# Optimization experiments

Measured on AMD Instinct MI355X. Metric: run time of the kernel, lower is better.

## Reference

```python
import jax, jax.numpy as jnp
import numpy as np

HEADS = 2

def gat_layer(x, edge_index, W, att, bias):
    # x: [N, Fin], W: [H*C, Fin], att: [1, H, 2C], bias: [C]
    N = x.shape[0]
    C = bias.shape[0]
    # add self loops (source_to_target: x_j from row 0, aggregate onto row 1)
    loop = jnp.arange(N, dtype=edge_index.dtype)
    src = jnp.concatenate([edge_index[0], loop])
    dst = jnp.concatenate([edge_index[1], loop])
    h = (x @ W.T).reshape(N, HEADS, C)          # [N, H, C]
    x_j = h[src]                                 # [E, H, C]
    x_i = h[dst]                                 # [E, H, C]
    x_cat = jnp.concatenate([x_i, x_j], axis=-1) # [E, H, 2C]
    alpha = (x_cat * att).sum(-1)                # [E, H]
    alpha = jnp.where(alpha >= 0, alpha, 0.2 * alpha)  # leaky_relu(0.2)
    # NOTE: module uses a global (not per-destination) normalization
    alpha = jnp.exp(alpha - alpha.max())
    alpha = alpha / (alpha.sum(axis=0, keepdims=True) + 1e-10)
    msg = x_j * alpha[..., None]                 # [E, H, C]
    aggr = jax.ops.segment_sum(msg, dst, num_segments=N)  # [N, H, C]
    return aggr.mean(axis=1) + bias              # [N, C]

def setup_inputs() -> dict:
    key = jax.random.key(0)
    ks = jax.random.split(key, 7)
    N, Fin, C = 50000, 128, 64
    E = 800000
    x = jax.random.normal(ks[0], (N, Fin), dtype=jnp.float32)
    edge_index = jax.random.randint(ks[1], (2, E), 0, N, dtype=jnp.int64)
    W1 = jax.random.normal(ks[2], (HEADS * C, Fin), dtype=jnp.float32) * 0.05
    att1 = jax.random.normal(ks[3], (1, HEADS, 2 * C), dtype=jnp.float32) * 0.05
    b1 = jnp.zeros((C,), dtype=jnp.float32)
    W2 = jax.random.normal(ks[4], (HEADS * C, C), dtype=jnp.float32) * 0.05
    att2 = jax.random.normal(ks[5], (1, HEADS, 2 * C), dtype=jnp.float32) * 0.05
    b2 = jnp.zeros((C,), dtype=jnp.float32)
    return {"x": x, "edge_index": edge_index, "W1": W1, "att1": att1,
            "b1": b1, "W2": W2, "att2": att2, "b2": b2}

def reference(x, edge_index, W1, att1, b1, W2, att2, b2):
    h = gat_layer(x, edge_index, W1, att1, b1)
    h = jax.nn.relu(h)
    # F.dropout with training flag: treated as eval (identity) for determinism
    out = gat_layer(h, edge_index, W2, att2, b2)
    return out
```

## Files before the change

kernel.cpp:

```cpp
#include <hip/hip_runtime.h>
#include <hip/hip_bf16.h>
#include <math.h>


#define HP 8
#define HG 64
#define NHISTB (HP * HG)
#define HRANGE_MAX 6272
#define NSELF 16
#define NWGT  256

using short8 = __attribute__((ext_vector_type(8))) short;
using f32x4  = __attribute__((ext_vector_type(4))) float;

__device__ __forceinline__ unsigned f2bf(float x) {
  unsigned u = __float_as_uint(x);
  return (u + 0x7fffu + ((u >> 16) & 1u)) >> 16;
}
__device__ __forceinline__ float bflo(unsigned p) { return __uint_as_float(p << 16); }
__device__ __forceinline__ float bfhi(unsigned p) { return __uint_as_float(p & 0xffff0000u); }
__device__ __forceinline__ float lrexp(float a) {
  a = a >= 0.f ? a : 0.2f * a;
  return __expf(a);
}

__device__ __forceinline__ void block_zadd(float z0, float z1,
                                           float* __restrict__ Zp) {
  __shared__ float r0[16], r1[16];
  int lane = threadIdx.x & 63, w = threadIdx.x >> 6;
  int nw = blockDim.x >> 6;
#pragma unroll
  for (int off = 32; off; off >>= 1) {
    z0 += __shfl_down(z0, off, 64);
    z1 += __shfl_down(z1, off, 64);
  }
  if (lane == 0) { r0[w] = z0; r1[w] = z1; }
  __syncthreads();
  if (threadIdx.x == 0) {
    float s0 = 0.f, s1 = 0.f;
    for (int i = 0; i < nw; ++i) { s0 += r0[i]; s1 += r1[i]; }
    atomicAdd(&Zp[0], s0);
    atomicAdd(&Zp[1], s1);
  }
}

__global__ __launch_bounds__(256) void init_ws(
    const float* __restrict__ W1, const float* __restrict__ W2,
    unsigned short* __restrict__ wbf1, unsigned short* __restrict__ wbf2,
    float* __restrict__ Z, int* __restrict__ flags) {
  int tid = blockIdx.x * 256 + threadIdx.x;
  int stride = gridDim.x * 256;
  for (int i = tid; i < 128 * 128; i += stride)
    wbf1[i] = (unsigned short)f2bf(W1[i]);
  for (int i = tid; i < 128 * 64; i += stride)
    wbf2[i] = (unsigned short)f2bf(W2[i]);
  if (tid < 4) Z[tid] = 0.f;
  if (tid < 64) flags[tid] = -1;
}

template <int FIN, bool AB16>
__global__ __launch_bounds__(256) void gemm_mfma(
    const void* __restrict__ xin, const unsigned short* __restrict__ Wb,
    const float* __restrict__ att, unsigned* __restrict__ hq,
    float* __restrict__ si, float* __restrict__ sj,
    int N,
    const int* __restrict__ dstE, unsigned short* __restrict__ partial,
    int E, int nhistb, int hstep, int eper) {
  const int tid = threadIdx.x;

  constexpr int WB = 128 * FIN * 2;
  constexpr int SMEM = (WB > HRANGE_MAX * 4) ? WB : HRANGE_MAX * 4;
  __shared__ __align__(16) unsigned char smem[SMEM];

  if ((int)blockIdx.x < nhistb) {
    int* lhist = (int*)smem;
    const int p = blockIdx.x & (HP - 1);
    const int g = blockIdx.x >> 3;
    const int lo = p * hstep;
    for (int i = tid; i < hstep; i += 256) lhist[i] = 0;
    __syncthreads();
    const int eb = g * eper;
    const int ee = min(E, eb + eper);
    int e = eb + tid;
    for (; e + 3 * 256 < ee; e += 4 * 256) {
      int d0 = dstE[e] - lo;
      int d1 = dstE[e + 256] - lo;
      int d2 = dstE[e + 2 * 256] - lo;
      int d3 = dstE[e + 3 * 256] - lo;
      if ((unsigned)d0 < (unsigned)hstep) atomicAdd(&lhist[d0], 1);
      if ((unsigned)d1 < (unsigned)hstep) atomicAdd(&lhist[d1], 1);
      if ((unsigned)d2 < (unsigned)hstep) atomicAdd(&lhist[d2], 1);
      if ((unsigned)d3 < (unsigned)hstep) atomicAdd(&lhist[d3], 1);
    }
    for (; e < ee; e += 256) {
      int d = dstE[e] - lo;
      if ((unsigned)d < (unsigned)hstep) atomicAdd(&lhist[d], 1);
    }
    __syncthreads();
    for (int i = tid; i < hstep; i += 256) {
      int node = lo + i;
      if (node < N) partial[(size_t)g * N + node] = (unsigned short)lhist[i];
    }
    return;
  }

  constexpr int KS = FIN / 32;
  constexpr int CPR = FIN / 8;
  constexpr int NCHUNK = 128 * CPR;

  unsigned short* wlds = (unsigned short*)smem;

  const int w    = tid >> 6;
  const int lane = tid & 63;
  const int cl   = lane & 15;
  const int grp  = lane >> 4;
  const int n0   = (blockIdx.x - nhistb) * 64;

  const int arow = n0 + w * 16 + cl;
  const bool avalid = arow < N;

  short8 afrag[KS];
#pragma unroll
  for (int ks = 0; ks < KS; ++ks) {
    if constexpr (AB16) {
      short8 z = {0, 0, 0, 0, 0, 0, 0, 0};
      afrag[ks] = z;
      if (avalid) {
        const unsigned short* xb = (const unsigned short*)xin;
        afrag[ks] =
            *(const short8*)(xb + (size_t)arow * FIN + ks * 32 + grp * 8);
      }
    } else {
      float4 v0 = make_float4(0.f, 0.f, 0.f, 0.f), v1 = v0;
      if (avalid) {
        const float* xf = (const float*)xin;
        const float4* xp =
            (const float4*)(xf + (size_t)arow * FIN + ks * 32 + grp * 8);
        v0 = xp[0];
        v1 = xp[1];
      }
      union { short8 s8; unsigned u[4]; } af;
      af.u[0] = f2bf(v0.x) | (f2bf(v0.y) << 16);
      af.u[1] = f2bf(v0.z) | (f2bf(v0.w) << 16);
      af.u[2] = f2bf(v1.x) | (f2bf(v1.y) << 16);
      af.u[3] = f2bf(v1.z) | (f2bf(v1.w) << 16);
      afrag[ks] = af.s8;
    }
  }

  const uint4* Wb4 = (const uint4*)Wb;
  for (int c = tid; c < NCHUNK; c += 256) {
    int row = c / CPR;
    int cc  = c & (CPR - 1);
    *(uint4*)&wlds[row * FIN + ((cc ^ (row & (CPR - 1))) * 8)] = Wb4[c];
  }
  __syncthreads();

  f32x4 acc[8];
#pragma unroll
  for (int ct = 0; ct < 8; ++ct) acc[ct] = (f32x4){0.f, 0.f, 0.f, 0.f};

  const int swz = cl & (CPR - 1);
#pragma unroll
  for (int ks = 0; ks < KS; ++ks) {
#pragma unroll
    for (int ct = 0; ct < 8; ++ct) {
      const unsigned short* bp =
          &wlds[(ct * 16 + cl) * FIN + (((ks * 4 + grp) ^ swz) * 8)];
      short8 bfrag = *(const short8*)bp;
      acc[ct] = __builtin_amdgcn_mfma_f32_16x16x32_bf16(afrag[ks], bfrag,
                                                        acc[ct], 0, 0, 0);
    }
  }

  float ai[8], aj[8];
#pragma unroll
  for (int ct = 0; ct < 8; ++ct) {
    int hd = ct >> 2;
    int cw = (ct & 3) * 16 + cl;
    ai[ct] = att[hd * 128 + cw];
    aj[ct] = att[hd * 128 + 64 + cw];
  }

#pragma unroll
  for (int r = 0; r < 4; ++r) {
    int node = n0 + w * 16 + grp * 4 + r;
    float s0i = 0.f, s0j = 0.f, s1i = 0.f, s1j = 0.f;
    unsigned wpk[4];
#pragma unroll
    for (int ct = 0; ct < 4; ++ct) {
      float v0 = acc[ct][r];
      float v1 = acc[ct + 4][r];
      s0i += v0 * ai[ct];
      s0j += v0 * aj[ct];
      s1i += v1 * ai[ct + 4];
      s1j += v1 * aj[ct + 4];
      wpk[ct] = f2bf(v0) | (f2bf(v1) << 16);
    }
#pragma unroll
    for (int off = 8; off; off >>= 1) {
      s0i += __shfl_xor(s0i, off, 64);
      s0j += __shfl_xor(s0j, off, 64);
      s1i += __shfl_xor(s1i, off, 64);
      s1j += __shfl_xor(s1j, off, 64);
    }
    if (node < N) {
#pragma unroll
      for (int ct = 0; ct < 4; ++ct)
        hq[(size_t)node * 64 + ct * 16 + cl] = wpk[ct];
      if (cl == 0) {
        si[node * 2 + 0] = s0i;
        si[node * 2 + 1] = s1i;
        sj[node * 2 + 0] = s0j;
        sj[node * 2 + 1] = s1j;
      }
    }
  }
}

__global__ __launch_bounds__(256) void scan_full(
    unsigned short* __restrict__ partial, int* __restrict__ rowptr,
    int* __restrict__ flags, int N, int Eall, int nb) {
  __shared__ int ts[256];
  __shared__ int pre_s;
  const int b = blockIdx.x, t = threadIdx.x;
  const int base = b * 1024 + t * 4;
  int r0 = 0, r1 = 0, r2 = 0, r3 = 0;
  if (base < N) {
#pragma unroll 8
    for (int g = 0; g < HG; ++g) {
      unsigned long long* p =
          (unsigned long long*)&partial[(size_t)g * N + base];
      unsigned long long v = *p;
      *p = (unsigned long long)(unsigned short)r0 |
           ((unsigned long long)(unsigned short)r1 << 16) |
           ((unsigned long long)(unsigned short)r2 << 32) |
           ((unsigned long long)(unsigned short)r3 << 48);
      r0 += (int)(v & 0xffffu);
      r1 += (int)((v >> 16) & 0xffffu);
      r2 += (int)((v >> 32) & 0xffffu);
      r3 += (int)((v >> 48) & 0xffffu);
    }
  }
  const int tot = r0 + r1 + r2 + r3;
  ts[t] = tot;
  __syncthreads();
#pragma unroll
  for (int off = 1; off < 256; off <<= 1) {
    int x = (t >= off) ? ts[t - off] : 0;
    __syncthreads();
    ts[t] += x;
    __syncthreads();
  }
  const int run_local = ts[t] - tot;
  const int blktot = ts[255];
  if (t == 0)
    __hip_atomic_store(&flags[b], blktot, __ATOMIC_RELEASE,
                       __HIP_MEMORY_SCOPE_AGENT);
  __syncthreads();
  if (t < b) {
    int v;
    do {
      v = __hip_atomic_load(&flags[t], __ATOMIC_ACQUIRE,
                            __HIP_MEMORY_SCOPE_AGENT);
    } while (v < 0);
    ts[t] = v;
  }
  __syncthreads();
  if (t == 0) {
    int acc = 0;
    for (int i = 0; i < b; ++i) acc += ts[i];
    pre_s = acc;
  }
  __syncthreads();
  int run = pre_s + run_local;
  if (base < N) {
    rowptr[base] = run;         run += r0;
    rowptr[base + 1] = run;     run += r1;
    rowptr[base + 2] = run;     run += r2;
    rowptr[base + 3] = run;
  }
  if (b == nb - 1 && t == 255) rowptr[N] = Eall;
}

__device__ __forceinline__ uint2 mkrec(int s, int d, float w0, float w1) {
  return make_uint2((unsigned)s | ((unsigned)d << 16),
                    f2bf(w0) | (f2bf(w1) << 16));
}

__global__ __launch_bounds__(1024) void scatter_z(
    const int* __restrict__ srcE, const int* __restrict__ dstE,
    const unsigned short* __restrict__ partial, const int* __restrict__ rowptr,
    uint2* __restrict__ erec,
    const float2* __restrict__ si2, const float2* __restrict__ sj2,
    float* __restrict__ Zp, int E, int hstep, int N, int eper) {
  __shared__ __align__(16) int lcur[HRANGE_MAX];
  const int tid = threadIdx.x;
  float z0 = 0.f, z1 = 0.f;

  if ((int)blockIdx.x < NSELF) {
    for (int n = blockIdx.x * 1024 + tid; n < N; n += NSELF * 1024) {
      float2 a = si2[n], b = sj2[n];
      z0 += lrexp(a.x + b.x);
      z1 += lrexp(a.y + b.y);
    }
    block_zadd(z0, z1, Zp);
    return;
  }

  const int bid = blockIdx.x - NSELF;
  const int p = bid & (HP - 1);
  const int g = bid >> 3;
  const int lo = p * hstep;
  for (int i = tid; i < hstep; i += 1024) {
    int node = lo + i;
    lcur[i] = (node < N)
                  ? rowptr[node] + (int)partial[(size_t)g * N + node]
                  : 0;
  }
  __syncthreads();

  const int eb = g * eper;
  const int ee = min(E, eb + eper);
  int e = eb + tid;
  for (; e + 3 * 1024 < ee; e += 4 * 1024) {
    int d0 = dstE[e], d1 = dstE[e + 1024];
    int d2 = dstE[e + 2 * 1024], d3 = dstE[e + 3 * 1024];
    int s0 = srcE[e], s1 = srcE[e + 1024];
    int s2 = srcE[e + 2 * 1024], s3 = srcE[e + 3 * 1024];
    int t0 = d0 - lo, t1 = d1 - lo, t2 = d2 - lo, t3 = d3 - lo;
    if ((unsigned)t0 < (unsigned)hstep) {
      float2 siv = si2[d0], sjv = sj2[s0];
      float w0 = lrexp(siv.x + sjv.x), w1 = lrexp(siv.y + sjv.y);
      z0 += w0; z1 += w1;
      erec[atomicAdd(&lcur[t0], 1)] = mkrec(s0, d0, w0, w1);
    }
    if ((unsigned)t1 < (unsigned)hstep) {
      float2 siv = si2[d1], sjv = sj2[s1];
      float w0 = lrexp(siv.x + sjv.x), w1 = lrexp(siv.y + sjv.y);
      z0 += w0; z1 += w1;
      erec[atomicAdd(&lcur[t1], 1)] = mkrec(s1, d1, w0, w1);
    }
    if ((unsigned)t2 < (unsigned)hstep) {
      float2 siv = si2[d2], sjv = sj2[s2];
      float w0 = lrexp(siv.x + sjv.x), w1 = lrexp(siv.y + sjv.y);
      z0 += w0; z1 += w1;
      erec[atomicAdd(&lcur[t2], 1)] = mkrec(s2, d2, w0, w1);
    }
    if ((unsigned)t3 < (unsigned)hstep) {
      float2 siv = si2[d3], sjv = sj2[s3];
      float w0 = lrexp(siv.x + sjv.x), w1 = lrexp(siv.y + sjv.y);
      z0 += w0; z1 += w1;
      erec[atomicAdd(&lcur[t3], 1)] = mkrec(s3, d3, w0, w1);
    }
  }
  for (; e < ee; e += 1024) {
    int d = dstE[e];
    int dd = d - lo;
    if ((unsigned)dd < (unsigned)hstep) {
      int s = srcE[e];
      float2 siv = si2[d], sjv = sj2[s];
      float w0 = lrexp(siv.x + sjv.x), w1 = lrexp(siv.y + sjv.y);
      z0 += w0; z1 += w1;
      erec[atomicAdd(&lcur[dd], 1)] = mkrec(s, d, w0, w1);
    }
  }
  block_zadd(z0, z1, Zp);
}

__global__ __launch_bounds__(1024) void z_wgt2(
    const float2* __restrict__ si2, const float2* __restrict__ sj2,
    float* __restrict__ Zp, uint2* __restrict__ erec, int E, int N) {
  const int tid = threadIdx.x;
  float z0 = 0.f, z1 = 0.f;
  if ((int)blockIdx.x < NSELF) {
    for (int n = blockIdx.x * 1024 + tid; n < N; n += NSELF * 1024) {
      float2 a = si2[n], b = sj2[n];
      z0 += lrexp(a.x + b.x);
      z1 += lrexp(a.y + b.y);
    }
  } else {
    int k = (blockIdx.x - NSELF) * 1024 + tid;
    for (; k < E; k += NWGT * 1024) {
      uint2 r = erec[k];
      int s = (int)(r.x & 0xffffu);
      int d = (int)(r.x >> 16);
      float2 siv = si2[d];
      float2 sjv = sj2[s];
      float w0 = lrexp(siv.x + sjv.x);
      float w1 = lrexp(siv.y + sjv.y);
      z0 += w0; z1 += w1;
      r.y = f2bf(w0) | (f2bf(w1) << 16);
      erec[k] = r;
    }
  }
  block_zadd(z0, z1, Zp);
}

__device__ __forceinline__ void edge8r(
    const uint2* __restrict__ erec, int k, const unsigned* __restrict__ hq,
    int lane, float& acc0, float& acc1) {
  uint2 r0 = erec[k],     r1 = erec[k + 1], r2 = erec[k + 2], r3 = erec[k + 3];
  uint2 r4 = erec[k + 4], r5 = erec[k + 5], r6 = erec[k + 6], r7 = erec[k + 7];
  unsigned p0 = hq[(size_t)(r0.x & 0xffffu) * 64 + lane];
  unsigned p1 = hq[(size_t)(r1.x & 0xffffu) * 64 + lane];
  unsigned p2 = hq[(size_t)(r2.x & 0xffffu) * 64 + lane];
  unsigned p3 = hq[(size_t)(r3.x & 0xffffu) * 64 + lane];
  unsigned p4 = hq[(size_t)(r4.x & 0xffffu) * 64 + lane];
  unsigned p5 = hq[(size_t)(r5.x & 0xffffu) * 64 + lane];
  unsigned p6 = hq[(size_t)(r6.x & 0xffffu) * 64 + lane];
  unsigned p7 = hq[(size_t)(r7.x & 0xffffu) * 64 + lane];
  acc0 = fmaf(bflo(p0), bflo(r0.y), acc0);  acc1 = fmaf(bfhi(p0), bfhi(r0.y), acc1);
  acc0 = fmaf(bflo(p1), bflo(r1.y), acc0);  acc1 = fmaf(bfhi(p1), bfhi(r1.y), acc1);
  acc0 = fmaf(bflo(p2), bflo(r2.y), acc0);  acc1 = fmaf(bfhi(p2), bfhi(r2.y), acc1);
  acc0 = fmaf(bflo(p3), bflo(r3.y), acc0);  acc1 = fmaf(bfhi(p3), bfhi(r3.y), acc1);
  acc0 = fmaf(bflo(p4), bflo(r4.y), acc0);  acc1 = fmaf(bfhi(p4), bfhi(r4.y), acc1);
  acc0 = fmaf(bflo(p5), bflo(r5.y), acc0);  acc1 = fmaf(bfhi(p5), bfhi(r5.y), acc1);
  acc0 = fmaf(bflo(p6), bflo(r6.y), acc0);  acc1 = fmaf(bfhi(p6), bfhi(r6.y), acc1);
  acc0 = fmaf(bflo(p7), bflo(r7.y), acc0);  acc1 = fmaf(bfhi(p7), bfhi(r7.y), acc1);
}
__device__ __forceinline__ void edge4r(
    const uint2* __restrict__ erec, int k, const unsigned* __restrict__ hq,
    int lane, float& acc0, float& acc1) {
  uint2 r0 = erec[k], r1 = erec[k + 1], r2 = erec[k + 2], r3 = erec[k + 3];
  unsigned p0 = hq[(size_t)(r0.x & 0xffffu) * 64 + lane];
  unsigned p1 = hq[(size_t)(r1.x & 0xffffu) * 64 + lane];
  unsigned p2 = hq[(size_t)(r2.x & 0xffffu) * 64 + lane];
  unsigned p3 = hq[(size_t)(r3.x & 0xffffu) * 64 + lane];
  acc0 = fmaf(bflo(p0), bflo(r0.y), acc0);  acc1 = fmaf(bfhi(p0), bfhi(r0.y), acc1);
  acc0 = fmaf(bflo(p1), bflo(r1.y), acc0);  acc1 = fmaf(bfhi(p1), bfhi(r1.y), acc1);
  acc0 = fmaf(bflo(p2), bflo(r2.y), acc0);  acc1 = fmaf(bfhi(p2), bfhi(r2.y), acc1);
  acc0 = fmaf(bflo(p3), bflo(r3.y), acc0);  acc1 = fmaf(bfhi(p3), bfhi(r3.y), acc1);
}
__device__ __forceinline__ void edge1r(
    int s, float w0, float w1, const unsigned* __restrict__ hq, int lane,
    float& acc0, float& acc1) {
  unsigned p = hq[(size_t)s * 64 + lane];
  acc0 = fmaf(bflo(p), w0, acc0);
  acc1 = fmaf(bfhi(p), w1, acc1);
}

__global__ __launch_bounds__(256) void csr_aggregate(
    const int* __restrict__ rowptr, const uint2* __restrict__ erec,
    const unsigned* __restrict__ hq, const float2* __restrict__ si2,
    const float2* __restrict__ sj2, const float* __restrict__ Zp,
    const float* __restrict__ bias, void* __restrict__ out,
    int N, int do_relu, int bf16_out) {
  int lane = threadIdx.x & 63;
  int wid = (blockIdx.x * blockDim.x + threadIdx.x) >> 6;
  int nw = (gridDim.x * blockDim.x) >> 6;
  float z0 = 1.f / (Zp[0] + 1e-10f);
  float z1 = 1.f / (Zp[1] + 1e-10f);
  float bv = bias[lane];
  for (int n0 = wid; n0 < N; n0 += nw) {
    int n = __builtin_amdgcn_readfirstlane(n0);
    int beg = rowptr[n], end = rowptr[n + 1];
    float2 siv = si2[n];
    float2 jv = sj2[n];
    float acc0 = 0.f, acc1 = 0.f;
    edge1r(n, lrexp(siv.x + jv.x), lrexp(siv.y + jv.y), hq, lane, acc0, acc1);
    int k = beg;
    for (; k + 8 <= end; k += 8) edge8r(erec, k, hq, lane, acc0, acc1);
    if (k + 4 <= end) { edge4r(erec, k, hq, lane, acc0, acc1); k += 4; }
    for (; k < end; ++k) {
      uint2 r = erec[k];
      edge1r((int)(r.x & 0xffffu), bflo(r.y), bfhi(r.y), hq, lane, acc0, acc1);
    }
    float r = 0.5f * (acc0 * z0 + acc1 * z1) + bv;
    if (do_relu) r = fmaxf(r, 0.f);
    if (bf16_out)
      ((unsigned short*)out)[(size_t)n * 64 + lane] = (unsigned short)f2bf(r);
    else
      ((float*)out)[(size_t)n * 64 + lane] = r;
  }
}

extern "C" void kernel_launch(void* const* d_in, const int* in_sizes, int n_in,
                              void* d_out, int out_size, void* d_ws, size_t ws_size,
                              hipStream_t stream) {
  const float* x    = (const float*)d_in[0];
  const int*   ei   = (const int*)d_in[1];
  const float* W1   = (const float*)d_in[2];
  const float* att1 = (const float*)d_in[3];
  const float* b1   = (const float*)d_in[4];
  const float* W2   = (const float*)d_in[5];
  const float* att2 = (const float*)d_in[6];
  const float* b2   = (const float*)d_in[7];
  float* out = (float*)d_out;

  const int N = in_sizes[0] / 128;
  const int E = in_sizes[1] / 2;
  const int* srcE = ei;
  const int* dstE = ei + E;

  unsigned* hq = (unsigned*)d_ws;
  float* si    = (float*)(hq + (size_t)N * 64);
  float* sj    = si + (size_t)N * 2;
  float* Z     = sj + (size_t)N * 2;
  float* x2    = Z + 4;
  unsigned short* partial = (unsigned short*)x2;
  unsigned short* x2b = (unsigned short*)x2;
  int* rowptr  = (int*)(x2 + (size_t)N * 64);
  int* flags   = rowptr + (N + 1);
  uintptr_t ep = ((uintptr_t)(flags + 64) + 15) & ~(uintptr_t)15;
  uint2* erec  = (uint2*)ep;
  unsigned short* wbf1 = (unsigned short*)(erec + E);
  unsigned short* wbf2 = wbf1 + 128 * 128;

  dim3 blk(256);
  dim3 blk1k(1024);
  int nb = (N + 1023) / 1024;
  int ntiles = (N + 63) / 64;
  int hstep = (N + HP - 1) / HP;
  int eper  = (E + HG - 1) / HG;

  init_ws<<<64, blk, 0, stream>>>(W1, W2, wbf1, wbf2, Z, flags);
  gemm_mfma<128, false><<<NHISTB + ntiles, blk, 0, stream>>>(
      x, wbf1, att1, hq, si, sj, N, dstE, partial, E, NHISTB, hstep, eper);
  scan_full<<<nb, blk, 0, stream>>>(partial, rowptr, flags, N, E, nb);
  scatter_z<<<NSELF + NHISTB, blk1k, 0, stream>>>(
      srcE, dstE, partial, rowptr, erec, (const float2*)si,
      (const float2*)sj, Z, E, hstep, N, eper);
  csr_aggregate<<<4096, blk, 0, stream>>>(rowptr, erec, hq,
                                          (const float2*)si, (const float2*)sj,
                                          Z, b1, x2b, N, 1, 1);
  gemm_mfma<64, true><<<ntiles, blk, 0, stream>>>(
      x2b, wbf2, att2, hq, si, sj, N, dstE, partial, E, 0, hstep, eper);
  z_wgt2<<<NSELF + NWGT, blk1k, 0, stream>>>(
      (const float2*)si, (const float2*)sj, Z + 2, erec, E, N);
  csr_aggregate<<<4096, blk, 0, stream>>>(rowptr, erec, hq,
                                          (const float2*)si, (const float2*)sj,
                                          Z + 2, b2, out, N, 0, 0);
}
```

Before: 232.5 us.

## Fold weight conversion and init into GEMM, software-pipeline CSR edge loads

Removes the separate init_ws kernel launch. Each GEMM block now converts fp32 weights to bf16 while staging them into LDS, and histogram block 0 zeroes Z and the scan flags. The CSR aggregation loop prefetches the next 8 edge records before using the current ones, to hide edge-record latency. The z_wgt2 grid grows from 256 to 496 blocks. The cost is redundant weight conversion in every GEMM tile and a dependence on block 0 finishing its init before the later kernels run, which stream ordering provides.

```diff
diff --git a/kernel.cpp b/kernel.cpp
--- a/kernel.cpp
+++ b/kernel.cpp
@@ -8,7 +8,7 @@
 #define NHISTB (HP * HG)
 #define HRANGE_MAX 6272
 #define NSELF 16
-#define NWGT  256
+#define NWGT  496
 
 using short8 = __attribute__((ext_vector_type(8))) short;
 using f32x4  = __attribute__((ext_vector_type(4))) float;
@@ -44,27 +44,14 @@
   }
 }
 
-__global__ __launch_bounds__(256) void init_ws(
-    const float* __restrict__ W1, const float* __restrict__ W2,
-    unsigned short* __restrict__ wbf1, unsigned short* __restrict__ wbf2,
-    float* __restrict__ Z, int* __restrict__ flags) {
-  int tid = blockIdx.x * 256 + threadIdx.x;
-  int stride = gridDim.x * 256;
-  for (int i = tid; i < 128 * 128; i += stride)
-    wbf1[i] = (unsigned short)f2bf(W1[i]);
-  for (int i = tid; i < 128 * 64; i += stride)
-    wbf2[i] = (unsigned short)f2bf(W2[i]);
-  if (tid < 4) Z[tid] = 0.f;
-  if (tid < 64) flags[tid] = -1;
-}
-
 template <int FIN, bool AB16>
 __global__ __launch_bounds__(256) void gemm_mfma(
-    const void* __restrict__ xin, const unsigned short* __restrict__ Wb,
+    const void* __restrict__ xin, const float* __restrict__ W,
     const float* __restrict__ att, unsigned* __restrict__ hq,
     float* __restrict__ si, float* __restrict__ sj,
     int N,
     const int* __restrict__ dstE, unsigned short* __restrict__ partial,
+    float* __restrict__ Z, int* __restrict__ flags,
     int E, int nhistb, int hstep, int eper) {
   const int tid = threadIdx.x;
 
@@ -73,6 +60,10 @@
   __shared__ __align__(16) unsigned char smem[SMEM];
 
   if ((int)blockIdx.x < nhistb) {
+    if (blockIdx.x == 0) {
+      if (tid < 4) Z[tid] = 0.f;
+      else if (tid < 68) flags[tid - 4] = -1;
+    }
     int* lhist = (int*)smem;
     const int p = blockIdx.x & (HP - 1);
     const int g = blockIdx.x >> 3;
@@ -148,11 +139,15 @@
     }
   }
 
-  const uint4* Wb4 = (const uint4*)Wb;
+  const float4* W4 = (const float4*)W;
   for (int c = tid; c < NCHUNK; c += 256) {
     int row = c / CPR;
     int cc  = c & (CPR - 1);
-    *(uint4*)&wlds[row * FIN + ((cc ^ (row & (CPR - 1))) * 8)] = Wb4[c];
+    float4 lo = W4[c * 2];
+    float4 hi = W4[c * 2 + 1];
+    *(uint4*)&wlds[row * FIN + ((cc ^ (row & (CPR - 1))) * 8)] = make_uint4(
+        f2bf(lo.x) | (f2bf(lo.y) << 16), f2bf(lo.z) | (f2bf(lo.w) << 16),
+        f2bf(hi.x) | (f2bf(hi.y) << 16), f2bf(hi.z) | (f2bf(hi.w) << 16));
   }
   __syncthreads();
 
@@ -397,28 +392,36 @@
   block_zadd(z0, z1, Zp);
 }
 
-__device__ __forceinline__ void edge8r(
-    const uint2* __restrict__ erec, int k, const unsigned* __restrict__ hq,
-    int lane, float& acc0, float& acc1) {
-  uint2 r0 = erec[k],     r1 = erec[k + 1], r2 = erec[k + 2], r3 = erec[k + 3];
-  uint2 r4 = erec[k + 4], r5 = erec[k + 5], r6 = erec[k + 6], r7 = erec[k + 7];
-  unsigned p0 = hq[(size_t)(r0.x & 0xffffu) * 64 + lane];
-  unsigned p1 = hq[(size_t)(r1.x & 0xffffu) * 64 + lane];
-  unsigned p2 = hq[(size_t)(r2.x & 0xffffu) * 64 + lane];
-  unsigned p3 = hq[(size_t)(r3.x & 0xffffu) * 64 + lane];
-  unsigned p4 = hq[(size_t)(r4.x & 0xffffu) * 64 + lane];
-  unsigned p5 = hq[(size_t)(r5.x & 0xffffu) * 64 + lane];
-  unsigned p6 = hq[(size_t)(r6.x & 0xffffu) * 64 + lane];
-  unsigned p7 = hq[(size_t)(r7.x & 0xffffu) * 64 + lane];
-  acc0 = fmaf(bflo(p0), bflo(r0.y), acc0);  acc1 = fmaf(bfhi(p0), bfhi(r0.y), acc1);
-  acc0 = fmaf(bflo(p1), bflo(r1.y), acc0);  acc1 = fmaf(bfhi(p1), bfhi(r1.y), acc1);
-  acc0 = fmaf(bflo(p2), bflo(r2.y), acc0);  acc1 = fmaf(bfhi(p2), bfhi(r2.y), acc1);
-  acc0 = fmaf(bflo(p3), bflo(r3.y), acc0);  acc1 = fmaf(bfhi(p3), bfhi(r3.y), acc1);
-  acc0 = fmaf(bflo(p4), bflo(r4.y), acc0);  acc1 = fmaf(bfhi(p4), bfhi(r4.y), acc1);
-  acc0 = fmaf(bflo(p5), bflo(r5.y), acc0);  acc1 = fmaf(bfhi(p5), bfhi(r5.y), acc1);
-  acc0 = fmaf(bflo(p6), bflo(r6.y), acc0);  acc1 = fmaf(bfhi(p6), bfhi(r6.y), acc1);
-  acc0 = fmaf(bflo(p7), bflo(r7.y), acc0);  acc1 = fmaf(bfhi(p7), bfhi(r7.y), acc1);
-}
+struct Rec8 { uint2 a, b, c, d, e, f, g, h; };
+
+__device__ __forceinline__ Rec8 load8(const uint2* __restrict__ erec, int k) {
+  Rec8 R;
+  R.a = erec[k];     R.b = erec[k + 1]; R.c = erec[k + 2]; R.d = erec[k + 3];
+  R.e = erec[k + 4]; R.f = erec[k + 5]; R.g = erec[k + 6]; R.h = erec[k + 7];
+  return R;
+}
+
+__device__ __forceinline__ void use8(
+    const Rec8& R, const unsigned* __restrict__ hq, int lane,
+    float& acc0, float& acc1) {
+  unsigned p0 = hq[(size_t)(R.a.x & 0xffffu) * 64 + lane];
+  unsigned p1 = hq[(size_t)(R.b.x & 0xffffu) * 64 + lane];
+  unsigned p2 = hq[(size_t)(R.c.x & 0xffffu) * 64 + lane];
+  unsigned p3 = hq[(size_t)(R.d.x & 0xffffu) * 64 + lane];
+  unsigned p4 = hq[(size_t)(R.e.x & 0xffffu) * 64 + lane];
+  unsigned p5 = hq[(size_t)(R.f.x & 0xffffu) * 64 + lane];
+  unsigned p6 = hq[(size_t)(R.g.x & 0xffffu) * 64 + lane];
+  unsigned p7 = hq[(size_t)(R.h.x & 0xffffu) * 64 + lane];
+  acc0 = fmaf(bflo(p0), bflo(R.a.y), acc0);  acc1 = fmaf(bfhi(p0), bfhi(R.a.y), acc1);
+  acc0 = fmaf(bflo(p1), bflo(R.b.y), acc0);  acc1 = fmaf(bfhi(p1), bfhi(R.b.y), acc1);
+  acc0 = fmaf(bflo(p2), bflo(R.c.y), acc0);  acc1 = fmaf(bfhi(p2), bfhi(R.c.y), acc1);
+  acc0 = fmaf(bflo(p3), bflo(R.d.y), acc0);  acc1 = fmaf(bfhi(p3), bfhi(R.d.y), acc1);
+  acc0 = fmaf(bflo(p4), bflo(R.e.y), acc0);  acc1 = fmaf(bfhi(p4), bfhi(R.e.y), acc1);
+  acc0 = fmaf(bflo(p5), bflo(R.f.y), acc0);  acc1 = fmaf(bfhi(p5), bfhi(R.f.y), acc1);
+  acc0 = fmaf(bflo(p6), bflo(R.g.y), acc0);  acc1 = fmaf(bfhi(p6), bfhi(R.g.y), acc1);
+  acc0 = fmaf(bflo(p7), bflo(R.h.y), acc0);  acc1 = fmaf(bfhi(p7), bfhi(R.h.y), acc1);
+}
+
 __device__ __forceinline__ void edge4r(
     const uint2* __restrict__ erec, int k, const unsigned* __restrict__ hq,
     int lane, float& acc0, float& acc1) {
@@ -460,7 +463,15 @@
     float acc0 = 0.f, acc1 = 0.f;
     edge1r(n, lrexp(siv.x + jv.x), lrexp(siv.y + jv.y), hq, lane, acc0, acc1);
     int k = beg;
-    for (; k + 8 <= end; k += 8) edge8r(erec, k, hq, lane, acc0, acc1);
+    if (k + 8 <= end) {
+      Rec8 R = load8(erec, k);
+      for (k += 8; k + 8 <= end; k += 8) {
+        Rec8 Rn = load8(erec, k);
+        use8(R, hq, lane, acc0, acc1);
+        R = Rn;
+      }
+      use8(R, hq, lane, acc0, acc1);
+    }
     if (k + 4 <= end) { edge4r(erec, k, hq, lane, acc0, acc1); k += 4; }
     for (; k < end; ++k) {
       uint2 r = erec[k];
@@ -504,8 +515,6 @@
   int* flags   = rowptr + (N + 1);
   uintptr_t ep = ((uintptr_t)(flags + 64) + 15) & ~(uintptr_t)15;
   uint2* erec  = (uint2*)ep;
-  unsigned short* wbf1 = (unsigned short*)(erec + E);
-  unsigned short* wbf2 = wbf1 + 128 * 128;
 
   dim3 blk(256);
   dim3 blk1k(1024);
@@ -514,9 +523,9 @@
   int hstep = (N + HP - 1) / HP;
   int eper  = (E + HG - 1) / HG;
 
-  init_ws<<<64, blk, 0, stream>>>(W1, W2, wbf1, wbf2, Z, flags);
   gemm_mfma<128, false><<<NHISTB + ntiles, blk, 0, stream>>>(
-      x, wbf1, att1, hq, si, sj, N, dstE, partial, E, NHISTB, hstep, eper);
+      x, W1, att1, hq, si, sj, N, dstE, partial, Z, flags,
+      E, NHISTB, hstep, eper);
   scan_full<<<nb, blk, 0, stream>>>(partial, rowptr, flags, N, E, nb);
   scatter_z<<<NSELF + NHISTB, blk1k, 0, stream>>>(
       srcE, dstE, partial, rowptr, erec, (const float2*)si,
@@ -525,7 +534,8 @@
                                           (const float2*)si, (const float2*)sj,
                                           Z, b1, x2b, N, 1, 1);
   gemm_mfma<64, true><<<ntiles, blk, 0, stream>>>(
-      x2b, wbf2, att2, hq, si, sj, N, dstE, partial, E, 0, hstep, eper);
+      x2b, W2, att2, hq, si, sj, N, dstE, partial, Z, flags,
+      E, 0, hstep, eper);
   z_wgt2<<<NSELF + NWGT, blk1k, 0, stream>>>(
       (const float2*)si, (const float2*)sj, Z + 2, erec, E, N);
   csr_aggregate<<<4096, blk, 0, stream>>>(rowptr, erec, hq,
```

Result: slower. 238.6 us (+2.6%).
